# Performance work log

Hardware: AMD Instinct MI355X
Metric: run time of the kernel (lower is better)

Reference implementation:

```python
import jax, jax.numpy as jnp
import numpy as np

B, S = 2, 2048
D_MODEL = 1024
N_HEADS = 16
N_VALUES = 8192
D_RETR = 128
MAX_POS = 2048


def setup_inputs() -> dict:
    key = jax.random.key(0)
    ks = jax.random.split(key, 10)
    s = 0.02
    return {
        "hidden_states": jax.random.normal(ks[0], (B, S, D_MODEL), jnp.float32),
        "attention_mask": jnp.ones((B, S), jnp.float32),
        "Wq": jax.random.normal(ks[1], (D_MODEL, D_MODEL), jnp.float32) * s,
        "bq": jnp.zeros((D_MODEL,), jnp.float32),
        "Wk": jax.random.normal(ks[2], (D_MODEL, D_MODEL), jnp.float32) * s,
        "bk": jnp.zeros((D_MODEL,), jnp.float32),
        # torch init is round(ones)=all ones; use random 0/1 so the per-head dynamic mask is exercised
        "dynamic_mask": jnp.round(jax.random.uniform(ks[3], (N_HEADS, MAX_POS), jnp.float32)),
        "Wvq": jax.random.normal(ks[4], (D_MODEL, D_RETR), jnp.float32) * s,
        "bvq": jnp.zeros((D_RETR,), jnp.float32),
        "v_keys": jax.random.normal(ks[5], (N_VALUES, D_RETR), jnp.float32) * s,
        "v_embed": jax.random.normal(ks[6], (N_VALUES, D_MODEL), jnp.float32) * s,
        "Wo": jax.random.normal(ks[7], (D_MODEL, D_MODEL), jnp.float32) * s,
        "bo": jnp.zeros((D_MODEL,), jnp.float32),
    }


def reference(hidden_states, attention_mask, Wq, bq, Wk, bk, dynamic_mask,
              Wvq, bvq, v_keys, v_embed, Wo, bo):
    b, s, d = hidden_states.shape
    h = dynamic_mask.shape[0]
    hd = d // h
    dtype = hidden_states.dtype
    min_d = jnp.finfo(dtype).min

    q = (hidden_states @ Wq + bq).reshape(b, s, h, hd).transpose(0, 2, 1, 3)  # [B,H,S,hd]
    k = (hidden_states @ Wk + bk).reshape(b, s, h, hd).transpose(0, 2, 1, 3)

    # inner_func: top-1 codebook value retrieval
    vq = hidden_states @ Wvq + bvq                      # [B,S,Dr]
    sim = jnp.einsum('bsr,nr->bsn', vq, v_keys)         # [B,S,Nv]
    idx = jnp.argmax(sim, axis=-1)                      # top-1 indices [B,S]
    v = hidden_states * v_embed[idx]                    # [B,S,D]
    v = v.reshape(b, s, h, hd).transpose(0, 2, 1, 3)    # [B,H,S,hd]

    # 4D causal mask fused with per-head dynamic mask and padding mask
    tgt = attention_mask.shape[-1]
    causal = jnp.where(jnp.arange(tgt)[None, :] > jnp.arange(s)[:, None],
                       min_d, jnp.array(0, dtype))[None, None]        # [1,1,S,S]
    am = attention_mask[:, None, None, :] * dynamic_mask[None, :, None, :tgt]  # [B,H,1,S]
    padding = causal + am                                              # [B,H,S,S]
    mask = jnp.where(padding == 0, min_d, causal)                      # [B,H,S,S]

    scores = jnp.einsum('bhqd,bhkd->bhqk', q, k) / jnp.sqrt(jnp.array(hd, dtype))
    scores = scores + mask
    w = jax.nn.softmax(scores.astype(jnp.float32), axis=-1).astype(dtype)

    out = jnp.einsum('bhqk,bhkd->bhqd', w, v)            # [B,H,S,hd]
    out = out.transpose(0, 2, 1, 3).reshape(b, s, d)
    return out @ Wo + bo
```

## Files before the change

### kernel.cpp

```cpp
#include <hip/hip_runtime.h>
#include <hip/hip_bf16.h>
#include <math.h>

#define MIN_D (-3.402823466e+38f)

constexpr int Bb = 2, Ss = 2048, Dm = 1024, Hh = 16, HDd = 64, NV = 8192, DRr = 128;
constexpr int Mrows = Bb * Ss;
constexpr float MARGIN = 0.01f;
constexpr int CAP = 262144;
constexpr float C2 = 0.18033688011112042f;

typedef __attribute__((ext_vector_type(8))) short bf16x8;
typedef __attribute__((ext_vector_type(4))) float f32x4;

__device__ inline unsigned short f2bf(float x) {
    union { float f; unsigned u; } v; v.f = x;
    unsigned r = v.u + 0x7fff + ((v.u >> 16) & 1);
    return (unsigned short)(r >> 16);
}
__device__ inline float bf2f(unsigned short u) {
    union { unsigned u; float f; } v; v.u = ((unsigned)u) << 16;
    return v.f;
}
__device__ inline unsigned pk_bf16(float a, float b) {
    float2 t; t.x = a; t.y = b;
    __hip_bfloat162 h = __float22bfloat162_rn(t);
    return *(unsigned*)&h;
}

__global__ __launch_bounds__(256)
void cvt_bf16(const float* __restrict__ x, unsigned short* __restrict__ y)
{
    size_t i = ((size_t)blockIdx.x * 256 + threadIdx.x) * 8;
    float4 a = *(const float4*)(x + i);
    float4 b = *(const float4*)(x + i + 4);
    uint4 p;
    p.x = pk_bf16(a.x, a.y);
    p.y = pk_bf16(a.z, a.w);
    p.z = pk_bf16(b.x, b.y);
    p.w = pk_bf16(b.z, b.w);
    *(uint4*)(y + i) = p;
}

__global__ __launch_bounds__(256)
void transpose_cvt3(const float* __restrict__ W0, const float* __restrict__ W1,
                    const float* __restrict__ W2, unsigned short* __restrict__ T0,
                    unsigned short* __restrict__ T1, unsigned short* __restrict__ T2)
{
    const float* W = blockIdx.z == 0 ? W0 : (blockIdx.z == 1 ? W1 : W2);
    unsigned short* WT = blockIdx.z == 0 ? T0 : (blockIdx.z == 1 ? T1 : T2);
    __shared__ unsigned short T[64][72];
    const int tid = threadIdx.x;
    const int n0 = blockIdx.x * 64, k0 = blockIdx.y * 64;
    const int rr = tid >> 4, cc = tid & 15;
#pragma unroll
    for (int q2 = 0; q2 < 4; ++q2) {
        int kk = rr * 4 + q2;
        float4 v = *(const float4*)(W + (size_t)(k0 + kk) * Dm + n0 + cc * 4);
        T[cc * 4 + 0][kk] = f2bf(v.x);
        T[cc * 4 + 1][kk] = f2bf(v.y);
        T[cc * 4 + 2][kk] = f2bf(v.z);
        T[cc * 4 + 3][kk] = f2bf(v.w);
    }
    __syncthreads();
#pragma unroll
    for (int q2 = 0; q2 < 4; ++q2) {
        int nn = rr * 4 + q2;
        uint2 u;
        u.x = (unsigned)T[nn][cc * 4 + 0] | ((unsigned)T[nn][cc * 4 + 1] << 16);
        u.y = (unsigned)T[nn][cc * 4 + 2] | ((unsigned)T[nn][cc * 4 + 3] << 16);
        *(uint2*)(WT + (size_t)(n0 + nn) * Dm + k0 + cc * 4) = u;
    }
}

template<bool BF16OUT>
__global__ __launch_bounds__(512)
void gemm_bf16(const unsigned short* __restrict__ A,
               const unsigned short* BT0, const unsigned short* BT1,
               const float* bias0, const float* bias1,
               void* C0, void* C1, int N, int K)
{
    const unsigned short* BT = blockIdx.z ? BT1 : BT0;
    const float* bias = blockIdx.z ? bias1 : bias0;
    void* C = blockIdx.z ? C1 : C0;
    __shared__ __align__(16) unsigned short As[128 * 32];
    __shared__ __align__(16) unsigned short Bs[128 * 32];
    const int tid = threadIdx.x;
    const int l = tid & 63, w = tid >> 6;
    const int l15 = l & 15, l4 = l >> 4;
    const int wm = w >> 2, wn = w & 3;
    const int row0 = blockIdx.y * 128, col0 = blockIdx.x * 128;

    f32x4 acc[4][2];
#pragma unroll
    for (int mi = 0; mi < 4; ++mi)
#pragma unroll
        for (int ni = 0; ni < 2; ++ni) acc[mi][ni] = (f32x4)(0.f);

    for (int k0 = 0; k0 < K; k0 += 32) {
        __syncthreads();
        {
            int r = tid >> 2, pc = tid & 3;
            uint4 vv = *(const uint4*)(A + (size_t)(row0 + r) * K + k0 + pc * 8);
            *(uint4*)&As[tid * 8] = vv;
        }
        {
            int r = tid >> 2, pc = tid & 3;
            uint4 vv = *(const uint4*)(BT + (size_t)(col0 + r) * K + k0 + pc * 8);
            *(uint4*)&Bs[tid * 8] = vv;
        }
        __syncthreads();

        bf16x8 af[4], bf[2];
#pragma unroll
        for (int mi = 0; mi < 4; ++mi)
            af[mi] = *(bf16x8*)&As[(wm * 64 + mi * 16 + l15) * 32 + l4 * 8];
#pragma unroll
        for (int ni = 0; ni < 2; ++ni)
            bf[ni] = *(bf16x8*)&Bs[(wn * 32 + ni * 16 + l15) * 32 + l4 * 8];
#pragma unroll
        for (int mi = 0; mi < 4; ++mi)
#pragma unroll
            for (int ni = 0; ni < 2; ++ni)
                acc[mi][ni] = __builtin_amdgcn_mfma_f32_16x16x32_bf16(af[mi], bf[ni], acc[mi][ni], 0, 0, 0);
    }

#pragma unroll
    for (int mi = 0; mi < 4; ++mi)
#pragma unroll
        for (int ni = 0; ni < 2; ++ni)
#pragma unroll
            for (int j = 0; j < 4; ++j) {
                int row = row0 + wm * 64 + mi * 16 + l4 * 4 + j;
                int col = col0 + wn * 32 + ni * 16 + l15;
                float vv = acc[mi][ni][j] + bias[col];
                if (BF16OUT)
                    ((unsigned short*)C)[(size_t)row * N + col] = f2bf(vv);
                else
                    ((float*)C)[(size_t)row * N + col] = vv;
            }
}

__global__ __launch_bounds__(256)
void gemm_vq_partial(const float* __restrict__ A, const float* __restrict__ W,
                     float* __restrict__ P)
{
    __shared__ float As[64][36];
    __shared__ float Ws[32][64];
    const int tid = threadIdx.x;
    const int row0 = blockIdx.y * 64, col0 = blockIdx.x * 64;
    const int kbase = blockIdx.z * 256;
    const int tr = tid >> 4, tc = tid & 15;
    float acc[4][4] = {};

    for (int k0 = kbase; k0 < kbase + 256; k0 += 32) {
        __syncthreads();
#pragma unroll
        for (int q2 = 0; q2 < 2; ++q2) {
            int oc = q2 * 256 + tid;
            int r = oc >> 3, c4 = (oc & 7) << 2;
            *(float4*)&As[r][c4] = *(const float4*)(A + (size_t)(row0 + r) * Dm + k0 + c4);
        }
#pragma unroll
        for (int q2 = 0; q2 < 2; ++q2) {
            int oc = q2 * 256 + tid;
            int r = oc >> 4, c4 = (oc & 15) << 2;
            *(float4*)&Ws[r][c4] = *(const float4*)(W + (size_t)(k0 + r) * DRr + col0 + c4);
        }
        __syncthreads();
#pragma unroll 8
        for (int kk = 0; kk < 32; ++kk) {
            float a[4];
#pragma unroll
            for (int i = 0; i < 4; ++i) a[i] = As[tr * 4 + i][kk];
            float4 bv = *(const float4*)&Ws[kk][tc * 4];
            float b[4] = {bv.x, bv.y, bv.z, bv.w};
#pragma unroll
            for (int i = 0; i < 4; ++i)
#pragma unroll
                for (int j = 0; j < 4; ++j)
                    acc[i][j] = fmaf(a[i], b[j], acc[i][j]);
        }
    }
    float* Pz = P + (size_t)blockIdx.z * Mrows * DRr;
#pragma unroll
    for (int i = 0; i < 4; ++i) {
        int r = row0 + tr * 4 + i;
        float4 ov = {acc[i][0], acc[i][1], acc[i][2], acc[i][3]};
        *(float4*)(Pz + (size_t)r * DRr + col0 + tc * 4) = ov;
    }
}

__global__ __launch_bounds__(256)
void reduce_vq(const float* __restrict__ P, const float* __restrict__ bias,
               float* __restrict__ vqb, unsigned short* __restrict__ vq_hi)
{
    const size_t i4 = ((size_t)blockIdx.x * 256 + threadIdx.x) * 4;
    const int col = (int)(i4 & 127);
    const size_t stride = (size_t)Mrows * DRr;
    float4 s = *(const float4*)(P + i4);
#pragma unroll
    for (int z = 1; z < 4; ++z) {
        float4 p = *(const float4*)(P + stride * z + i4);
        s.x += p.x; s.y += p.y; s.z += p.z; s.w += p.w;
    }
    float4 bv = *(const float4*)(bias + col);
    s.x += bv.x; s.y += bv.y; s.z += bv.z; s.w += bv.w;
    *(float4*)(vqb + i4) = s;
    uint2 u;
    u.x = pk_bf16(s.x, s.y);
    u.y = pk_bf16(s.z, s.w);
    *(uint2*)(vq_hi + i4) = u;
}

template<int PASS>
__global__ __launch_bounds__(512)
void sim_gemm(const unsigned short* __restrict__ A,
              const unsigned short* __restrict__ BT,
              float* __restrict__ rowtilemax, const float* __restrict__ thr,
              unsigned* __restrict__ cnt, unsigned* __restrict__ pairs)
{
    __shared__ __align__(16) unsigned short As[128 * 32];
    __shared__ __align__(16) unsigned short Bs[128 * 32];
    __shared__ float red[128][4];
    __shared__ float thrsm[128];
    const int tid = threadIdx.x;
    const int l = tid & 63, w = tid >> 6;
    const int l15 = l & 15, l4 = l >> 4;
    const int wm = w >> 2, wn = w & 3;
    const int row0 = blockIdx.y * 128, col0 = blockIdx.x * 128;

    if (PASS == 1 && tid < 128) thrsm[tid] = thr[row0 + tid];

    f32x4 acc[4][2];
#pragma unroll
    for (int mi = 0; mi < 4; ++mi)
#pragma unroll
        for (int ni = 0; ni < 2; ++ni) acc[mi][ni] = (f32x4)(0.f);

    for (int k0 = 0; k0 < DRr; k0 += 32) {
        __syncthreads();
        {
            int r = tid >> 2, pc = tid & 3;
            uint4 vv = *(const uint4*)(A + (size_t)(row0 + r) * DRr + k0 + pc * 8);
            *(uint4*)&As[tid * 8] = vv;
        }
        {
            int r = tid >> 2, pc = tid & 3;
            uint4 vv = *(const uint4*)(BT + (size_t)(col0 + r) * DRr + k0 + pc * 8);
            *(uint4*)&Bs[tid * 8] = vv;
        }
        __syncthreads();

        bf16x8 af[4], bf[2];
#pragma unroll
        for (int mi = 0; mi < 4; ++mi)
            af[mi] = *(bf16x8*)&As[(wm * 64 + mi * 16 + l15) * 32 + l4 * 8];
#pragma unroll
        for (int ni = 0; ni < 2; ++ni)
            bf[ni] = *(bf16x8*)&Bs[(wn * 32 + ni * 16 + l15) * 32 + l4 * 8];
#pragma unroll
        for (int mi = 0; mi < 4; ++mi)
#pragma unroll
            for (int ni = 0; ni < 2; ++ni)
                acc[mi][ni] = __builtin_amdgcn_mfma_f32_16x16x32_bf16(af[mi], bf[ni], acc[mi][ni], 0, 0, 0);
    }

    if (PASS == 0) {
        float rm[4][4];
#pragma unroll
        for (int mi = 0; mi < 4; ++mi)
#pragma unroll
            for (int j = 0; j < 4; ++j)
                rm[mi][j] = fmaxf(acc[mi][0][j], acc[mi][1][j]);
#pragma unroll
        for (int off = 1; off < 16; off <<= 1)
#pragma unroll
            for (int mi = 0; mi < 4; ++mi)
#pragma unroll
                for (int j = 0; j < 4; ++j)
                    rm[mi][j] = fmaxf(rm[mi][j], __shfl_xor(rm[mi][j], off));
        if (l15 == 0) {
#pragma unroll
            for (int mi = 0; mi < 4; ++mi)
#pragma unroll
                for (int j = 0; j < 4; ++j)
                    red[wm * 64 + mi * 16 + l4 * 4 + j][wn] = rm[mi][j];
        }
        __syncthreads();
        if (tid < 128) {
            float m = fmaxf(fmaxf(red[tid][0], red[tid][1]),
                            fmaxf(red[tid][2], red[tid][3]));
            rowtilemax[(size_t)(row0 + tid) * 64 + blockIdx.x] = m;
        }
    } else {
        __syncthreads();
#pragma unroll
        for (int mi = 0; mi < 4; ++mi)
#pragma unroll
            for (int ni = 0; ni < 2; ++ni)
#pragma unroll
                for (int j = 0; j < 4; ++j) {
                    const int rl = wm * 64 + mi * 16 + l4 * 4 + j;
                    if (acc[mi][ni][j] >= thrsm[rl]) {
                        const int col = col0 + wn * 32 + ni * 16 + l15;
                        unsigned slot = atomicAdd(cnt, 1u);
                        if (slot < (unsigned)CAP)
                            pairs[slot] = ((unsigned)(row0 + rl) << 13) | (unsigned)col;
                    }
                }
    }
}

__global__ __launch_bounds__(256)
void sim_combine2(const float* __restrict__ rtm, float* __restrict__ thr)
{
    int r = blockIdx.x * 256 + threadIdx.x;
    if (r >= Mrows) return;
    const float4* p = (const float4*)(rtm + (size_t)r * 64);
    float m = -INFINITY;
#pragma unroll
    for (int c = 0; c < 16; ++c) {
        float4 v = p[c];
        m = fmaxf(m, fmaxf(fmaxf(v.x, v.y), fmaxf(v.z, v.w)));
    }
    thr[r] = m - MARGIN;
}

__global__ __launch_bounds__(256)
void sim_rescore(const unsigned* __restrict__ pairs, const unsigned* __restrict__ cnt,
                 const float* __restrict__ vq, const float* __restrict__ vkeys,
                 unsigned long long* __restrict__ best)
{
    const int l = threadIdx.x & 63;
    const unsigned wav = (blockIdx.x * 256 + threadIdx.x) >> 6;
    const unsigned nw = (gridDim.x * 256) >> 6;
    const unsigned n = min(*cnt, (unsigned)CAP);
    for (unsigned i = wav; i < n; i += nw) {
        unsigned p = pairs[i];
        unsigned row = p >> 13, key = p & 8191u;
        float2 a = *(const float2*)(vq + (size_t)row * 128 + l * 2);
        float2 b = *(const float2*)(vkeys + (size_t)key * 128 + l * 2);
        float d = a.x * b.x + a.y * b.y;
#pragma unroll
        for (int off = 32; off; off >>= 1) d += __shfl_xor(d, off);
        if (l == 0) {
            unsigned fb = __float_as_uint(d);
            fb = (fb & 0x80000000u) ? ~fb : (fb | 0x80000000u);
            unsigned long long enc = ((unsigned long long)fb << 32) | (unsigned)(~key);
            atomicMax(best + row, enc);
        }
    }
}

__global__ __launch_bounds__(256)
void build_vt(const float* __restrict__ hs, const float* __restrict__ vembed,
              const unsigned long long* __restrict__ best,
              unsigned short* __restrict__ vt)
{
    __shared__ unsigned short T[64][73];
    __shared__ int ids[64];
    const int tid = threadIdx.x;
    const int kt = blockIdx.x;
    const int bh = blockIdx.y;
    const int b = bh >> 4, h = bh & 15;
    if (tid < 64) {
        int row = b * Ss + kt * 64 + tid;
        ids[tid] = (int)((~(unsigned)(best[row] & 0xFFFFFFFFull)) & 8191u);
    }
    __syncthreads();
    {
        int r = tid >> 2, c16 = (tid & 3) * 16;
        size_t hrow = (size_t)(b * Ss + kt * 64 + r) * Dm + h * HDd + c16;
        size_t erow = (size_t)ids[r] * Dm + h * HDd + c16;
#pragma unroll
        for (int q2 = 0; q2 < 4; ++q2) {
            float4 a = *(const float4*)(hs + hrow + q2 * 4);
            float4 e = *(const float4*)(vembed + erow + q2 * 4);
            T[r][c16 + q2 * 4 + 0] = f2bf(a.x * e.x);
            T[r][c16 + q2 * 4 + 1] = f2bf(a.y * e.y);
            T[r][c16 + q2 * 4 + 2] = f2bf(a.z * e.z);
            T[r][c16 + q2 * 4 + 3] = f2bf(a.w * e.w);
        }
    }
    __syncthreads();
    {
        int d = tid >> 2, kc = (tid & 3) * 16;
        unsigned short ob[16];
#pragma unroll
        for (int i = 0; i < 16; ++i) ob[i] = T[kc + i][d];
        unsigned short* op = vt + ((size_t)(b * Hh + h) * HDd + d) * Ss + kt * 64 + kc;
        *(uint4*)op = *(uint4*)&ob[0];
        *(uint4*)(op + 8) = *(uint4*)&ob[8];
    }
}

__global__ __launch_bounds__(256)
void mean_vt(const unsigned short* __restrict__ vt, float* __restrict__ mv)
{
    const int bh = blockIdx.x;
    const int b = bh >> 4, h = bh & 15;
    const int d = threadIdx.x >> 2, part = threadIdx.x & 3;
    const unsigned short* row = vt + ((size_t)bh * HDd + d) * Ss + part * 512;
    float s = 0.f;
    for (int j = 0; j < 512; j += 8) {
        uint4 u = *(const uint4*)(row + j);
        const unsigned uu[4] = {u.x, u.y, u.z, u.w};
#pragma unroll
        for (int m = 0; m < 4; ++m) {
            s += bf2f((unsigned short)(uu[m] & 0xffff));
            s += bf2f((unsigned short)(uu[m] >> 16));
        }
    }
    s += __shfl_xor(s, 1);
    s += __shfl_xor(s, 2);
    if (part == 0) mv[b * Dm + h * HDd + d] = s * (1.f / 2048.f);
}

__global__ __launch_bounds__(512)
void attn_mfma4(const unsigned short* __restrict__ q, const unsigned short* __restrict__ k,
                const unsigned short* __restrict__ vt, const float* __restrict__ am,
                const float* __restrict__ dmask, const float* __restrict__ meanv,
                unsigned short* __restrict__ o)
{
    __shared__ __align__(16) unsigned char smem[40960];
    __shared__ float uniflag[128];
    unsigned char* Ksm = smem;
    unsigned char* Vsm = smem + 8192;
    unsigned char* Psm = smem + 16384;
    float* amdmf = (float*)(smem + 32768);

    const int tid = threadIdx.x;
    const int l = tid & 63, w = tid >> 6;
    const int l15 = l & 15, l4 = l >> 4;
    const int lin = blockIdx.x + (blockIdx.y << 4) + (blockIdx.z << 8);
    const int half = lin >> 8, rem = lin & 255;
    const int qtb = rem & 15;
    const int qt = half ? (15 - qtb) : qtb;
    const int h = rem >> 4;
    const int b = half;
    const int row0 = qt * 128;

    {
        int j = tid * 4;
        float4 a = *(const float4*)(am + b * Ss + j);
        float4 d = *(const float4*)(dmask + h * Ss + j);
        float4 m;
        m.x = (a.x * d.x == 0.f) ? MIN_D : 0.f;
        m.y = (a.y * d.y == 0.f) ? MIN_D : 0.f;
        m.z = (a.z * d.z == 0.f) ? MIN_D : 0.f;
        m.w = (a.w * d.w == 0.f) ? MIN_D : 0.f;
        *(float4*)&amdmf[j] = m;
    }

    const int qloc = w * 16 + l15;
    const int qrow = row0 + qloc;
    bf16x8 qf[2];
    {
        const unsigned short* qp = q + ((size_t)(b * Ss + qrow)) * Dm + h * HDd + l4 * 8;
        qf[0] = *(const bf16x8*)qp;
        qf[1] = *(const bf16x8*)(qp + 32);
    }

    f32x4 acc[4];
#pragma unroll
    for (int d2 = 0; d2 < 4; ++d2) acc[d2] = (f32x4)(0.f);
    float mrun = -INFINITY, lrun = 0.f;
    const int ktmax = 2 * qt + 1;

    for (int kt = 0; kt <= ktmax; ++kt) {
        __syncthreads();
        {
            int key = tid >> 3, pc = tid & 7, lc = pc ^ (key & 7);
            uint4 vv = *(const uint4*)(k + ((size_t)(b * Ss + kt * 64 + key)) * Dm
                                       + h * HDd + lc * 8);
            *(uint4*)&Ksm[tid * 16] = vv;
        }
        {
            int d = tid >> 3, pc = tid & 7, lc = pc ^ (d & 7);
            uint4 vv = *(const uint4*)(vt + ((size_t)(b * Hh + h) * HDd + d) * Ss
                                       + kt * 64 + lc * 8);
            *(uint4*)&Vsm[tid * 16] = vv;
        }
        __syncthreads();

        f32x4 sreg[4];
#pragma unroll
        for (int kb = 0; kb < 4; ++kb) {
            const int key16 = kb * 16 + l15;
            const int sw = key16 & 7;
            bf16x8 k0 = *(bf16x8*)&Ksm[key16 * 128 + ((l4 ^ sw) * 16)];
            bf16x8 k1 = *(bf16x8*)&Ksm[key16 * 128 + (((4 + l4) ^ sw) * 16)];
            f32x4 s = (f32x4)(0.f);
            s = __builtin_amdgcn_mfma_f32_16x16x32_bf16(k0, qf[0], s, 0, 0, 0);
            s = __builtin_amdgcn_mfma_f32_16x16x32_bf16(k1, qf[1], s, 0, 0, 0);
            sreg[kb] = s;
        }

        float sv[16];
#pragma unroll
        for (int kb = 0; kb < 4; ++kb)
#pragma unroll
            for (int r = 0; r < 4; ++r) {
                const int key = kt * 64 + kb * 16 + l4 * 4 + r;
                const float mval = (key > qrow) ? MIN_D : amdmf[key];
                sv[kb * 4 + r] = fmaf(sreg[kb][r], C2, mval);
            }

        float pm = fmaxf(fmaxf(sv[0], sv[1]), sv[2]);
        pm = fmaxf(fmaxf(pm, sv[3]), fmaxf(sv[4], sv[5]));
        pm = fmaxf(fmaxf(pm, sv[6]), fmaxf(sv[7], sv[8]));
        pm = fmaxf(fmaxf(pm, sv[9]), fmaxf(sv[10], sv[11]));
        pm = fmaxf(fmaxf(pm, sv[12]), fmaxf(sv[13], sv[14]));
        pm = fmaxf(pm, sv[15]);
        pm = fmaxf(pm, __shfl_xor(pm, 16));
        pm = fmaxf(pm, __shfl_xor(pm, 32));

        if (__any(pm > mrun + 8.f)) {
            const float mn = fmaxf(mrun, pm);
            const float sc = __builtin_amdgcn_exp2f(mrun - mn);
            lrun *= sc;
#pragma unroll
            for (int d2 = 0; d2 < 4; ++d2) acc[d2] *= sc;
            mrun = mn;
        }

        float p[16], rs = 0.f;
#pragma unroll
        for (int i = 0; i < 16; ++i) {
            p[i] = __builtin_amdgcn_exp2f(sv[i] - mrun);
            rs += p[i];
        }
        rs += __shfl_xor(rs, 16);
        rs += __shfl_xor(rs, 32);
        lrun += rs;

        const unsigned pswz = (l15 & 7) << 4;
#pragma unroll
        for (int kb = 0; kb < 4; ++kb) {
            uint2 u;
            u.x = pk_bf16(p[kb * 4 + 0], p[kb * 4 + 1]);
            u.y = pk_bf16(p[kb * 4 + 2], p[kb * 4 + 3]);
            *(uint2*)&Psm[qloc * 128 + ((kb * 32 + l4 * 8) ^ pswz)] = u;
        }

#pragma unroll
        for (int ks = 0; ks < 2; ++ks) {
            bf16x8 pa = *(bf16x8*)&Psm[qloc * 128 + ((ks * 64 + l4 * 16) ^ pswz)];
#pragma unroll
            for (int d2 = 0; d2 < 4; ++d2) {
                const int dd = d2 * 16 + l15;
                bf16x8 vb = *(bf16x8*)&Vsm[dd * 128 + ((ks * 64 + l4 * 16) ^ ((dd & 7) << 4))];
                acc[d2] = __builtin_amdgcn_mfma_f32_16x16x32_bf16(vb, pa, acc[d2], 0, 0, 0);
            }
        }
    }

    const float inv = 1.f / lrun;
    const bool uni = (mrun <= -1e37f);
    __syncthreads();
    unsigned short* stg = (unsigned short*)smem;
    uniflag[qloc] = uni ? 1.f : 0.f;
#pragma unroll
    for (int d2 = 0; d2 < 4; ++d2) {
        uint2 u;
        u.x = pk_bf16(acc[d2][0] * inv, acc[d2][1] * inv);
        u.y = pk_bf16(acc[d2][2] * inv, acc[d2][3] * inv);
        *(uint2*)&stg[qloc * 72 + d2 * 16 + l4 * 4] = u;
    }
    __syncthreads();
    {
        const int r = tid >> 2, c16 = (tid & 3) * 16;
        const bool u = uniflag[r] != 0.f;
        uint4 o0, o1;
        if (u) {
            unsigned short ob[16];
#pragma unroll
            for (int i = 0; i < 16; ++i)
                ob[i] = f2bf(meanv[b * Dm + h * HDd + c16 + i]);
            o0 = *(uint4*)&ob[0];
            o1 = *(uint4*)&ob[8];
        } else {
            o0 = *(uint4*)&stg[r * 72 + c16];
            o1 = *(uint4*)&stg[r * 72 + c16 + 8];
        }
        unsigned short* op = o + ((size_t)(b * Ss + row0 + r)) * Dm + h * HDd + c16;
        *(uint4*)op = o0;
        *(uint4*)(op + 8) = o1;
    }
}

extern "C" void kernel_launch(void* const* d_in, const int* in_sizes, int n_in,
                              void* d_out, int out_size, void* d_ws, size_t ws_size,
                              hipStream_t stream)
{
    const float* hs     = (const float*)d_in[0];
    const float* amask  = (const float*)d_in[1];
    const float* Wq     = (const float*)d_in[2];
    const float* bq     = (const float*)d_in[3];
    const float* Wk     = (const float*)d_in[4];
    const float* bk     = (const float*)d_in[5];
    const float* dmask  = (const float*)d_in[6];
    const float* Wvq    = (const float*)d_in[7];
    const float* bvq    = (const float*)d_in[8];
    const float* vkeys  = (const float*)d_in[9];
    const float* vembed = (const float*)d_in[10];
    const float* Wo     = (const float*)d_in[11];
    const float* bo     = (const float*)d_in[12];
    float* out = (float*)d_out;

    char* w = (char*)d_ws;
    size_t off = 0;
    auto take = [&](size_t n) { char* p = w + off; off = (off + n + 255) & ~(size_t)255; return p; };
    unsigned short* hsbf  = (unsigned short*)take((size_t)Mrows * Dm * 2);
    unsigned short* WqT   = (unsigned short*)take((size_t)Dm * Dm * 2);
    unsigned short* WkT   = (unsigned short*)take((size_t)Dm * Dm * 2);
    unsigned short* WoT   = (unsigned short*)take((size_t)Dm * Dm * 2);
    unsigned short* qbf   = (unsigned short*)take((size_t)Mrows * Dm * 2);
    unsigned short* kbf   = (unsigned short*)take((size_t)Mrows * Dm * 2);
    unsigned short* vtb   = (unsigned short*)take((size_t)Mrows * Dm * 2);
    unsigned short* attno = (unsigned short*)take((size_t)Mrows * Dm * 2);
    float* vqp   = (float*)take((size_t)4 * Mrows * DRr * 4);
    float* vqb   = (float*)take((size_t)Mrows * DRr * 4);
    unsigned short* vq_hi = (unsigned short*)take((size_t)Mrows * DRr * 2);
    unsigned short* vk_hi = (unsigned short*)take((size_t)NV * DRr * 2);
    float* rtm   = (float*)take((size_t)Mrows * 64 * 4);
    float* thr   = (float*)take((size_t)Mrows * 4);
    unsigned* cnt = (unsigned*)take(256);
    unsigned* pairs = (unsigned*)take((size_t)CAP * 4);
    unsigned long long* best = (unsigned long long*)take((size_t)Mrows * 8);
    float* mvb   = (float*)take((size_t)Bb * Dm * 4);

    hipMemsetAsync(cnt, 0, 4, stream);
    hipMemsetAsync(best, 0, (size_t)Mrows * 8, stream);

    dim3 blk(256);
    cvt_bf16<<<dim3(Mrows * Dm / 2048), blk, 0, stream>>>(hs, hsbf);
    transpose_cvt3<<<dim3(Dm / 64, Dm / 64, 3), blk, 0, stream>>>(Wq, Wk, Wo, WqT, WkT, WoT);
    gemm_bf16<true><<<dim3(Dm / 128, Mrows / 128, 2), dim3(512), 0, stream>>>(
        hsbf, WqT, WkT, bq, bk, qbf, kbf, Dm, Dm);
    gemm_vq_partial<<<dim3(DRr / 64, Mrows / 64, 4), blk, 0, stream>>>(hs, Wvq, vqp);
    reduce_vq<<<dim3(Mrows * DRr / 1024), blk, 0, stream>>>(vqp, bvq, vqb, vq_hi);
    cvt_bf16<<<dim3(NV * DRr / 2048), blk, 0, stream>>>(vkeys, vk_hi);
    sim_gemm<0><<<dim3(NV / 128, Mrows / 128), dim3(512), 0, stream>>>(
        vq_hi, vk_hi, rtm, nullptr, nullptr, nullptr);
    sim_combine2<<<dim3(Mrows / 256), blk, 0, stream>>>(rtm, thr);
    sim_gemm<1><<<dim3(NV / 128, Mrows / 128), dim3(512), 0, stream>>>(
        vq_hi, vk_hi, nullptr, thr, cnt, pairs);
    sim_rescore<<<dim3(256), blk, 0, stream>>>(pairs, cnt, vqb, vkeys, best);
    build_vt<<<dim3(Ss / 64, Bb * Hh), blk, 0, stream>>>(hs, vembed, best, vtb);
    mean_vt<<<dim3(Bb * Hh), blk, 0, stream>>>(vtb, mvb);
    attn_mfma4<<<dim3(Ss / 128, Hh, Bb), dim3(512), 0, stream>>>(
        qbf, kbf, vtb, amask, dmask, mvb, attno);
    gemm_bf16<false><<<dim3(Dm / 128, Mrows / 128, 1), dim3(512), 0, stream>>>(
        attno, WoT, WoT, bo, bo, out, out, Dm, Dm);
}
```

Baseline: 277.4 us.

## Replace second sim GEMM pass with per-tile exact FP32 rescoring of candidates

Removes the second bf16 similarity GEMM pass, the global atomic pair list and the rescore kernel. Each 128-key tile now scans the per-tile row maxima against the threshold, builds a local candidate row list and rescores the whole tile in FP32 from LDS. The tile max layout is transposed so these scans read contiguously, and the first-pass GEMM loads its A and B tiles with direct global-to-LDS loads. The exact kernel runs only 64 blocks and loops over candidates serially with barriers, so its cost depends on how many rows fall within the margin.

```diff
diff --git a/kernel.cpp b/kernel.cpp
--- a/kernel.cpp
+++ b/kernel.cpp
@@ -7,7 +7,6 @@
 constexpr int Bb = 2, Ss = 2048, Dm = 1024, Hh = 16, HDd = 64, NV = 8192, DRr = 128;
 constexpr int Mrows = Bb * Ss;
 constexpr float MARGIN = 0.01f;
-constexpr int CAP = 262144;
 constexpr float C2 = 0.18033688011112042f;
 
 typedef __attribute__((ext_vector_type(8))) short bf16x8;
@@ -213,25 +212,20 @@
     *(uint2*)(vq_hi + i4) = u;
 }
 
-template<int PASS>
 __global__ __launch_bounds__(512)
-void sim_gemm(const unsigned short* __restrict__ A,
-              const unsigned short* __restrict__ BT,
-              float* __restrict__ rowtilemax, const float* __restrict__ thr,
-              unsigned* __restrict__ cnt, unsigned* __restrict__ pairs)
+void sim_gemm0(const unsigned short* __restrict__ A,
+               const unsigned short* __restrict__ BT,
+               float* __restrict__ rtm)
 {
     __shared__ __align__(16) unsigned short As[128 * 32];
     __shared__ __align__(16) unsigned short Bs[128 * 32];
     __shared__ float red[128][4];
-    __shared__ float thrsm[128];
     const int tid = threadIdx.x;
     const int l = tid & 63, w = tid >> 6;
     const int l15 = l & 15, l4 = l >> 4;
     const int wm = w >> 2, wn = w & 3;
     const int row0 = blockIdx.y * 128, col0 = blockIdx.x * 128;
 
-    if (PASS == 1 && tid < 128) thrsm[tid] = thr[row0 + tid];
-
     f32x4 acc[4][2];
 #pragma unroll
     for (int mi = 0; mi < 4; ++mi)
@@ -242,13 +236,12 @@
         __syncthreads();
         {
             int r = tid >> 2, pc = tid & 3;
-            uint4 vv = *(const uint4*)(A + (size_t)(row0 + r) * DRr + k0 + pc * 8);
-            *(uint4*)&As[tid * 8] = vv;
-        }
-        {
-            int r = tid >> 2, pc = tid & 3;
-            uint4 vv = *(const uint4*)(BT + (size_t)(col0 + r) * DRr + k0 + pc * 8);
-            *(uint4*)&Bs[tid * 8] = vv;
+            __builtin_amdgcn_global_load_lds(
+                (const __attribute__((address_space(1))) unsigned int*)(A + (size_t)(row0 + r) * DRr + k0 + pc * 8),
+                (__attribute__((address_space(3))) unsigned int*)&As[tid * 8], 16, 0, 0);
+            __builtin_amdgcn_global_load_lds(
+                (const __attribute__((address_space(1))) unsigned int*)(BT + (size_t)(col0 + r) * DRr + k0 + pc * 8),
+                (__attribute__((address_space(3))) unsigned int*)&Bs[tid * 8], 16, 0, 0);
         }
         __syncthreads();
 
@@ -266,49 +259,31 @@
                 acc[mi][ni] = __builtin_amdgcn_mfma_f32_16x16x32_bf16(af[mi], bf[ni], acc[mi][ni], 0, 0, 0);
     }
 
-    if (PASS == 0) {
-        float rm[4][4];
+    float rm[4][4];
+#pragma unroll
+    for (int mi = 0; mi < 4; ++mi)
+#pragma unroll
+        for (int j = 0; j < 4; ++j)
+            rm[mi][j] = fmaxf(acc[mi][0][j], acc[mi][1][j]);
+#pragma unroll
+    for (int off = 1; off < 16; off <<= 1)
 #pragma unroll
         for (int mi = 0; mi < 4; ++mi)
 #pragma unroll
             for (int j = 0; j < 4; ++j)
-                rm[mi][j] = fmaxf(acc[mi][0][j], acc[mi][1][j]);
-#pragma unroll
-        for (int off = 1; off < 16; off <<= 1)
-#pragma unroll
-            for (int mi = 0; mi < 4; ++mi)
-#pragma unroll
-                for (int j = 0; j < 4; ++j)
-                    rm[mi][j] = fmaxf(rm[mi][j], __shfl_xor(rm[mi][j], off));
-        if (l15 == 0) {
-#pragma unroll
-            for (int mi = 0; mi < 4; ++mi)
-#pragma unroll
-                for (int j = 0; j < 4; ++j)
-                    red[wm * 64 + mi * 16 + l4 * 4 + j][wn] = rm[mi][j];
-        }
-        __syncthreads();
-        if (tid < 128) {
-            float m = fmaxf(fmaxf(red[tid][0], red[tid][1]),
-                            fmaxf(red[tid][2], red[tid][3]));
-            rowtilemax[(size_t)(row0 + tid) * 64 + blockIdx.x] = m;
-        }
-    } else {
-        __syncthreads();
+                rm[mi][j] = fmaxf(rm[mi][j], __shfl_xor(rm[mi][j], off));
+    if (l15 == 0) {
 #pragma unroll
         for (int mi = 0; mi < 4; ++mi)
 #pragma unroll
-            for (int ni = 0; ni < 2; ++ni)
-#pragma unroll
-                for (int j = 0; j < 4; ++j) {
-                    const int rl = wm * 64 + mi * 16 + l4 * 4 + j;
-                    if (acc[mi][ni][j] >= thrsm[rl]) {
-                        const int col = col0 + wn * 32 + ni * 16 + l15;
-                        unsigned slot = atomicAdd(cnt, 1u);
-                        if (slot < (unsigned)CAP)
-                            pairs[slot] = ((unsigned)(row0 + rl) << 13) | (unsigned)col;
-                    }
-                }
+            for (int j = 0; j < 4; ++j)
+                red[wm * 64 + mi * 16 + l4 * 4 + j][wn] = rm[mi][j];
+    }
+    __syncthreads();
+    if (tid < 128) {
+        float m = fmaxf(fmaxf(red[tid][0], red[tid][1]),
+                        fmaxf(red[tid][2], red[tid][3]));
+        rtm[(size_t)blockIdx.x * Mrows + row0 + tid] = m;
     }
 }
 
@@ -317,39 +292,81 @@
 {
     int r = blockIdx.x * 256 + threadIdx.x;
     if (r >= Mrows) return;
-    const float4* p = (const float4*)(rtm + (size_t)r * 64);
     float m = -INFINITY;
-#pragma unroll
-    for (int c = 0; c < 16; ++c) {
-        float4 v = p[c];
-        m = fmaxf(m, fmaxf(fmaxf(v.x, v.y), fmaxf(v.z, v.w)));
-    }
+#pragma unroll 8
+    for (int c = 0; c < 64; ++c)
+        m = fmaxf(m, rtm[(size_t)c * Mrows + r]);
     thr[r] = m - MARGIN;
 }
 
 __global__ __launch_bounds__(256)
-void sim_rescore(const unsigned* __restrict__ pairs, const unsigned* __restrict__ cnt,
-                 const float* __restrict__ vq, const float* __restrict__ vkeys,
-                 unsigned long long* __restrict__ best)
-{
-    const int l = threadIdx.x & 63;
-    const unsigned wav = (blockIdx.x * 256 + threadIdx.x) >> 6;
-    const unsigned nw = (gridDim.x * 256) >> 6;
-    const unsigned n = min(*cnt, (unsigned)CAP);
-    for (unsigned i = wav; i < n; i += nw) {
-        unsigned p = pairs[i];
-        unsigned row = p >> 13, key = p & 8191u;
-        float2 a = *(const float2*)(vq + (size_t)row * 128 + l * 2);
-        float2 b = *(const float2*)(vkeys + (size_t)key * 128 + l * 2);
-        float d = a.x * b.x + a.y * b.y;
-#pragma unroll
-        for (int off = 32; off; off >>= 1) d += __shfl_xor(d, off);
-        if (l == 0) {
-            unsigned fb = __float_as_uint(d);
-            fb = (fb & 0x80000000u) ? ~fb : (fb | 0x80000000u);
-            unsigned long long enc = ((unsigned long long)fb << 32) | (unsigned)(~key);
-            atomicMax(best + row, enc);
-        }
+void sim_exact(const float* __restrict__ rtm, const float* __restrict__ thr,
+               const float* __restrict__ vq, const float* __restrict__ vkeys,
+               unsigned long long* __restrict__ best)
+{
+    __shared__ float vkt[128][129];
+    __shared__ float vqs[128];
+    __shared__ float part[256];
+    __shared__ int list[4096];
+    __shared__ int lcnt;
+    const int tid = threadIdx.x;
+    const int tile = blockIdx.x;
+    if (tid == 0) lcnt = 0;
+
+#pragma unroll
+    for (int i = 0; i < 16; ++i) {
+        int idx = i * 256 + tid;
+        int k = idx >> 5, d4 = (idx & 31) * 4;
+        float4 v = *(const float4*)(vkeys + (size_t)(tile * 128 + k) * 128 + d4);
+        vkt[d4 + 0][k] = v.x;
+        vkt[d4 + 1][k] = v.y;
+        vkt[d4 + 2][k] = v.z;
+        vkt[d4 + 3][k] = v.w;
+    }
+    __syncthreads();
+
+    for (int r = tid; r < Mrows; r += 256)
+        if (rtm[(size_t)tile * Mrows + r] >= thr[r]) {
+            int p = atomicAdd(&lcnt, 1);
+            list[p] = r;
+        }
+    __syncthreads();
+    const int n = lcnt;
+
+    for (int i = 0; i < n; ++i) {
+        const int row = list[i];
+        if (tid < 32) {
+            float4 v = *(const float4*)(vq + (size_t)row * 128 + tid * 4);
+            *(float4*)&vqs[tid * 4] = v;
+        }
+        __syncthreads();
+        const int k = tid & 127, h = (tid >> 7) * 64;
+        float s = 0.f;
+#pragma unroll
+        for (int d = 0; d < 64; ++d)
+            s = fmaf(vqs[h + d], vkt[h + d][k], s);
+        part[tid] = s;
+        __syncthreads();
+        if (tid < 64) {
+            float s0 = part[tid] + part[tid + 128];
+            float s1 = part[tid + 64] + part[tid + 192];
+            float bs = s0; int bk = tid;
+            if (s1 > s0) { bs = s1; bk = tid + 64; }
+#pragma unroll
+            for (int off = 1; off < 64; off <<= 1) {
+                float os = __shfl_xor(bs, off);
+                int ok = __shfl_xor(bk, off);
+                if (os > bs || (os == bs && ok < bk)) { bs = os; bk = ok; }
+            }
+            if (tid == 0) {
+                unsigned key = tile * 128 + bk;
+                unsigned fb = __float_as_uint(bs);
+                fb = (fb & 0x80000000u) ? ~fb : (fb | 0x80000000u);
+                unsigned long long enc = ((unsigned long long)fb << 32) | (unsigned)(~key);
+                atomicMax(best + row, enc);
+            }
+        }
+        __syncthreads();
     }
 }
 
@@ -624,14 +641,11 @@
     float* vqb   = (float*)take((size_t)Mrows * DRr * 4);
     unsigned short* vq_hi = (unsigned short*)take((size_t)Mrows * DRr * 2);
     unsigned short* vk_hi = (unsigned short*)take((size_t)NV * DRr * 2);
-    float* rtm   = (float*)take((size_t)Mrows * 64 * 4);
+    float* rtm   = (float*)take((size_t)64 * Mrows * 4);
     float* thr   = (float*)take((size_t)Mrows * 4);
-    unsigned* cnt = (unsigned*)take(256);
-    unsigned* pairs = (unsigned*)take((size_t)CAP * 4);
     unsigned long long* best = (unsigned long long*)take((size_t)Mrows * 8);
     float* mvb   = (float*)take((size_t)Bb * Dm * 4);
 
-    hipMemsetAsync(cnt, 0, 4, stream);
     hipMemsetAsync(best, 0, (size_t)Mrows * 8, stream);
 
     dim3 blk(256);
@@ -642,12 +656,9 @@
     gemm_vq_partial<<<dim3(DRr / 64, Mrows / 64, 4), blk, 0, stream>>>(hs, Wvq, vqp);
     reduce_vq<<<dim3(Mrows * DRr / 1024), blk, 0, stream>>>(vqp, bvq, vqb, vq_hi);
     cvt_bf16<<<dim3(NV * DRr / 2048), blk, 0, stream>>>(vkeys, vk_hi);
-    sim_gemm<0><<<dim3(NV / 128, Mrows / 128), dim3(512), 0, stream>>>(
-        vq_hi, vk_hi, rtm, nullptr, nullptr, nullptr);
+    sim_gemm0<<<dim3(NV / 128, Mrows / 128), dim3(512), 0, stream>>>(vq_hi, vk_hi, rtm);
     sim_combine2<<<dim3(Mrows / 256), blk, 0, stream>>>(rtm, thr);
-    sim_gemm<1><<<dim3(NV / 128, Mrows / 128), dim3(512), 0, stream>>>(
-        vq_hi, vk_hi, nullptr, thr, cnt, pairs);
-    sim_rescore<<<dim3(256), blk, 0, stream>>>(pairs, cnt, vqb, vkeys, best);
+    sim_exact<<<dim3(NV / 128), blk, 0, stream>>>(rtm, thr, vqb, vkeys, best);
     build_vt<<<dim3(Ss / 64, Bb * Hh), blk, 0, stream>>>(hs, vembed, best, vtb);
     mean_vt<<<dim3(Bb * Hh), blk, 0, stream>>>(vtb, mvb);
     attn_mfma4<<<dim3(Ss / 128, Hh, Bb), dim3(512), 0, stream>>>(
```

Measured after the change: 389.4 us. 40.4% more time.
